# Performance work log

Measured on AMD Instinct MI355X. Metric: run time of the kernel, lower is better.

The kernel has to match this reference:

```python
import jax, jax.numpy as jnp
import numpy as np

N, H, W, C = 8, 64, 64, 256  # C//4 = 64 query channels, HW = 4096 attention size


def setup_inputs() -> dict:
    key = jax.random.key(0)
    k1, k2, k3, k4 = jax.random.split(key, 4)
    src_mask = jax.random.uniform(k1, (N, H, W), dtype=jnp.float32)
    src_feature = jax.random.normal(k2, (N, H, W, C), dtype=jnp.float32)
    ref_feature = jax.random.normal(k3, (N, H, W, C), dtype=jnp.float32)
    w_query = jax.random.normal(k4, (C, C // 4), dtype=jnp.float32) * 0.02  # 1x1 conv weight
    return {"src_mask": src_mask, "src_feature": src_feature,
            "ref_feature": ref_feature, "w_query": w_query}


def _apply_attention_map(att_map, features):
    n, h, w, c = features.shape
    pixels = features.reshape(n, h * w, c).transpose(0, 2, 1)  # (N, C, HW)
    att_out = jnp.einsum('ncp,npq->ncq', pixels, att_map)      # (N, C, HW)
    return att_out.reshape(n, h, w, c)


def reference(src_mask, src_feature, ref_feature, w_query):
    n, h, w, c = src_feature.shape
    # 1x1 conv (no bias): per-pixel channel projection C -> C//4
    query = jnp.einsum('nhwc,cd->nhwd', src_feature, w_query).reshape(n, h * w, -1)
    # full (HW x HW) attention map, softmax over keys
    att_map = jax.nn.softmax(jnp.einsum('npd,nqd->npq', query, query), axis=-1)
    # original module applies the map to src_feature twice (src_att and ref_att)
    att_out = _apply_attention_map(att_map, src_feature)
    src_att = att_out
    ref_att = att_out
    m = src_mask[..., None]  # (N, H, W, 1)
    ex_guide_flow = m * ref_att + (1.0 - m) * ref_feature
    return jnp.concatenate([ex_guide_flow, src_att], axis=-1)  # (N, H, W, 2C)
```

## Files before the change

kernel.cpp:

```cpp
#include <hip/hip_runtime.h>

typedef unsigned short u16;
typedef unsigned int u32;
typedef __attribute__((ext_vector_type(8))) __bf16 bf16x8;
typedef __attribute__((ext_vector_type(8))) _Float16 f16x8;
typedef __attribute__((ext_vector_type(4))) float f32x4;

__device__ __forceinline__ float b2f(u16 b) {
    union { u32 u; float f; } v; v.u = ((u32)b) << 16; return v.f;
}
__device__ __forceinline__ u16 f2bf(float f) {
    union { float f; u32 u; } v; v.f = f;
    u32 u = v.u;
    return (u16)((u + 0x7fffu + ((u >> 16) & 1u)) >> 16);
}
__device__ __forceinline__ u16 f2h(float f) {
    _Float16 h = (_Float16)f;
    return __builtin_bit_cast(u16, h);
}
__device__ __forceinline__ u32 pkbf2(float a, float b) {
    u16 x = __builtin_bit_cast(u16, (__bf16)a);
    u16 y = __builtin_bit_cast(u16, (__bf16)b);
    return (u32)x | ((u32)y << 16);
}
__device__ __forceinline__ bf16x8 ldg8b(const u16* p) {
    uint4 v = *(const uint4*)p;
    return __builtin_bit_cast(bf16x8, v);
}
__device__ __forceinline__ f16x8 ldg8h(const u16* p) {
    uint4 v = *(const uint4*)p;
    return __builtin_bit_cast(f16x8, v);
}
__device__ __forceinline__ f32x4 mfma_bf(bf16x8 a, bf16x8 b, f32x4 c) {
    return __builtin_amdgcn_mfma_f32_16x16x32_bf16(a, b, c, 0, 0, 0);
}
__device__ __forceinline__ f32x4 mfma_h(f16x8 a, f16x8 b, f32x4 c) {
    return __builtin_amdgcn_mfma_f32_16x16x32_f16(a, b, c, 0, 0, 0);
}

#define LOG2E 1.44269504088896340736f


__global__ void k0_wt(const float* __restrict__ Wq,
                      u16* __restrict__ Wthi, u16* __restrict__ Wtlo) {
    int idx = blockIdx.x * 256 + threadIdx.x;
    int c = idx >> 6, d = idx & 63;
    float w = Wq[idx];
    u16 hi = f2bf(w);
    float rem = w - b2f(hi);
    Wthi[d * 256 + c] = hi;
    Wtlo[d * 256 + c] = f2bf(rem);
}

__global__ __launch_bounds__(256) void k1_query(
    const float* __restrict__ F, const u16* __restrict__ Wthi,
    const u16* __restrict__ Wtlo, u16* __restrict__ Qh) {
    const int t = threadIdx.x;
    const int w = t >> 6, L = t & 63, lane16 = L & 15, quad = L >> 4;
    const int R0 = blockIdx.x * 64;
    const int row = R0 + w * 16 + lane16;
    const f32x4 z4 = {0.f, 0.f, 0.f, 0.f};
    f32x4 acc[4] = {z4, z4, z4, z4};
    union U8 { bf16x8 v; u16 s[8]; };
#pragma unroll
    for (int ks = 0; ks < 8; ++ks) {
        const float* fp = F + (size_t)row * 256 + ks * 32 + quad * 8;
        float4 x0 = *(const float4*)fp;
        float4 x1 = *(const float4*)(fp + 4);
        float xs[8] = {x0.x, x0.y, x0.z, x0.w, x1.x, x1.y, x1.z, x1.w};
        U8 ahi, alo;
#pragma unroll
        for (int j = 0; j < 8; ++j) {
            u16 h = f2bf(xs[j]);
            ahi.s[j] = h;
            alo.s[j] = f2bf(xs[j] - b2f(h));
        }
#pragma unroll
        for (int nt = 0; nt < 4; ++nt) {
            const int off = (nt * 16 + lane16) * 256 + ks * 32 + quad * 8;
            bf16x8 bh = ldg8b(Wthi + off);
            bf16x8 bl = ldg8b(Wtlo + off);
            acc[nt] = mfma_bf(ahi.v, bh, acc[nt]);
            acc[nt] = mfma_bf(alo.v, bh, acc[nt]);
            acc[nt] = mfma_bf(ahi.v, bl, acc[nt]);
        }
    }
    const int orow = R0 + w * 16 + quad * 4;
#pragma unroll
    for (int nt = 0; nt < 4; ++nt) {
        const int d = nt * 16 + lane16;
#pragma unroll
        for (int r = 0; r < 4; ++r) {
            const int p = orow + r;
            Qh[(size_t)p * 64 + (d ^ ((p & 7) << 3))] = f2h(acc[nt][r]);
        }
    }
}

__global__ __launch_bounds__(256) void k2_suminv(
    const u16* __restrict__ Q, float* __restrict__ lgl) {
    const int t = threadIdx.x;
    const int w = t >> 6, L = t & 63, lane16 = L & 15, quad = L >> 4, l7 = lane16 & 7;
    const int bx = blockIdx.x;
    const int n = bx & 7, pb = bx >> 3;
    const int P0 = pb * 32;
    const u16* Qn = Q + (size_t)n * 4096 * 64;

    f16x8 ap[2][2];
#pragma unroll
    for (int st = 0; st < 2; ++st) {
        const int row = P0 + st * 16 + lane16;
        ap[st][0] = ldg8h(Qn + row * 64 + ((quad * 8) ^ (l7 * 8)));
        ap[st][1] = ldg8h(Qn + row * 64 + ((32 + quad * 8) ^ (l7 * 8)));
    }
    float sums[2][4];
#pragma unroll
    for (int st = 0; st < 2; ++st)
#pragma unroll
        for (int r = 0; r < 4; ++r) sums[st][r] = 0.f;

    const f32x4 z4 = {0.f, 0.f, 0.f, 0.f};
    for (int s = 0; s < 32; ++s) {
#pragma unroll
        for (int nt = 0; nt < 2; ++nt) {
            const int qr = w * 1024 + s * 32 + nt * 16 + lane16;
            f16x8 b0 = ldg8h(Qn + qr * 64 + ((quad * 8) ^ (l7 * 8)));
            f16x8 b1 = ldg8h(Qn + qr * 64 + ((32 + quad * 8) ^ (l7 * 8)));
#pragma unroll
            for (int st = 0; st < 2; ++st) {
                f32x4 z = z4;
                z = mfma_h(ap[st][0], b0, z);
                z = mfma_h(ap[st][1], b1, z);
                sums[st][0] += __expf(z[0]);
                sums[st][1] += __expf(z[1]);
                sums[st][2] += __expf(z[2]);
                sums[st][3] += __expf(z[3]);
            }
        }
    }
    __shared__ float red[4][32];
#pragma unroll
    for (int st = 0; st < 2; ++st)
#pragma unroll
        for (int r = 0; r < 4; ++r) {
            float v = sums[st][r];
            v += __shfl_xor(v, 1);
            v += __shfl_xor(v, 2);
            v += __shfl_xor(v, 4);
            v += __shfl_xor(v, 8);
            if (lane16 == 0) red[w][st * 16 + quad * 4 + r] = v;
        }
    __syncthreads();
    if (t < 32) {
        float tot = red[0][t] + red[1][t] + red[2][t] + red[3][t];
        lgl[n * 4096 + P0 + t] = -__log2f(tot);
    }
}

__global__ __launch_bounds__(256) void k3_gt(
    const float* __restrict__ F, u16* __restrict__ Gt) {
    const int t = threadIdx.x;
    const int bx = blockIdx.x;
    const int n = bx >> 6, s = bx & 63;
    const int p0 = s * 64;
    __shared__ float tile[64][65];
    const float* Fn = F + (size_t)n * 4096 * 256;
    u16* Gn = Gt + (size_t)(n * 64 + s) * 16384;
#pragma unroll 1
    for (int ct = 0; ct < 4; ++ct) {
        const int c0 = ct * 64;
        if (ct > 0) __syncthreads();
#pragma unroll
        for (int k = 0; k < 16; ++k) {
            int idx = k * 256 + t;
            int r = idx >> 6, cc = idx & 63;
            tile[r][cc] = Fn[(size_t)(p0 + r) * 256 + c0 + cc];
        }
        __syncthreads();
#pragma unroll
        for (int k = 0; k < 2; ++k) {
            int u = k * 256 + t;
            int cc = u & 63, S = u >> 6;
            int G = S ^ (cc & 7);
            u16 v[8];
#pragma unroll
            for (int j = 0; j < 8; ++j) v[j] = f2bf(tile[G * 8 + j][cc]);
            uint4 pk;
            pk.x = (u32)v[0] | ((u32)v[1] << 16);
            pk.y = (u32)v[2] | ((u32)v[3] << 16);
            pk.z = (u32)v[4] | ((u32)v[5] << 16);
            pk.w = (u32)v[6] | ((u32)v[7] << 16);
            *(uint4*)&Gn[(c0 + cc) * 64 + S * 8] = pk;
        }
    }
}

__global__ __launch_bounds__(256, 2) void k4_attn(
    const u16* __restrict__ Q, const u16* __restrict__ Gt,
    const float* __restrict__ lgl, const float* __restrict__ mask,
    const float* __restrict__ ref, float* __restrict__ out) {
    const int t = threadIdx.x;
    const int w = t >> 6, L = t & 63, lane16 = L & 15, quad = L >> 4, l7 = lane16 & 7;
    const int bx = blockIdx.x;
    const int n = bx & 7, qb = bx >> 3;
    const int q0 = qb << 6;

    __shared__ u16 sP[2][4096];

    const u16* Qn = Q + (size_t)n * 4096 * 64;
    const u16* Gtn = Gt + (size_t)n * 64 * 16384;
    const float* iln = lgl + n * 4096;

    f16x8 bq[4][2];
#pragma unroll
    for (int qt = 0; qt < 4; ++qt) {
        const int row = q0 + qt * 16 + lane16;
        bq[qt][0] = ldg8h(Qn + row * 64 + ((quad * 8) ^ (l7 * 8)));
        bq[qt][1] = ldg8h(Qn + row * 64 + ((32 + quad * 8) ^ (l7 * 8)));
    }

    const int sAg0 = (w * 16 + lane16) * 64 + ((quad * 8) ^ (l7 * 8));
    const int sAg1 = (w * 16 + lane16) * 64 + ((32 + quad * 8) ^ (l7 * 8));
    int wrP[4];
#pragma unroll
    for (int qt = 0; qt < 4; ++qt)
        wrP[qt] = (qt * 16 + lane16) * 64 +
                  ((w * 16 + 8 * (quad >> 1)) ^ (l7 * 8)) + 4 * (quad & 1);
    int rdP[4][2], sOf[4][2];
#pragma unroll
    for (int m = 0; m < 4; ++m)
#pragma unroll
        for (int h = 0; h < 2; ++h)
            rdP[m][h] = (m * 16 + lane16) * 64 + ((h * 32 + quad * 8) ^ (l7 * 8));
#pragma unroll
    for (int nt = 0; nt < 4; ++nt)
#pragma unroll
        for (int h = 0; h < 2; ++h)
            sOf[nt][h] = (w * 64 + nt * 16 + lane16) * 64 + ((h * 32 + quad * 8) ^ (l7 * 8));

    const f32x4 z4 = {0.f, 0.f, 0.f, 0.f};
    f32x4 acc[4][4];
#pragma unroll
    for (int a = 0; a < 4; ++a)
#pragma unroll
        for (int b = 0; b < 4; ++b) acc[a][b] = z4;

    f16x8 na0, na1;
    float4 nil4;
    bf16x8 bbA[8], bbB[8];

    auto s_phase = [&](f16x8 a0, f16x8 a1, float4 il4, u16* dst) {
        float lg0 = il4.x, lg1 = il4.y, lg2 = il4.z, lg3 = il4.w;
#pragma unroll
        for (int qt = 0; qt < 4; ++qt) {
            f32x4 z = z4;
            z = mfma_h(a0, bq[qt][0], z);
            z = mfma_h(a1, bq[qt][1], z);
            uint2 pk;
            pk.x = pkbf2(__builtin_exp2f(__builtin_fmaf(z[0], LOG2E, lg0)),
                         __builtin_exp2f(__builtin_fmaf(z[1], LOG2E, lg1)));
            pk.y = pkbf2(__builtin_exp2f(__builtin_fmaf(z[2], LOG2E, lg2)),
                         __builtin_exp2f(__builtin_fmaf(z[3], LOG2E, lg3)));
            *(uint2*)&dst[wrP[qt]] = pk;
        }
    };
    auto load_bb = [&](const u16* gstep, bf16x8* bb) {
#pragma unroll
        for (int h = 0; h < 2; ++h)
#pragma unroll
            for (int nt = 0; nt < 4; ++nt)
                bb[h * 4 + nt] = ldg8b(gstep + sOf[nt][h]);
    };
    auto pv_phase = [&](const u16* sPc, const bf16x8* bb) {
        __builtin_amdgcn_s_setprio(1);
#pragma unroll
        for (int h = 0; h < 2; ++h) {
            bf16x8 af[4];
#pragma unroll
            for (int m = 0; m < 4; ++m) af[m] = ldg8b(&sPc[rdP[m][h]]);
#pragma unroll
            for (int nt = 0; nt < 4; ++nt)
#pragma unroll
                for (int m = 0; m < 4; ++m)
                    acc[m][nt] = mfma_bf(af[m], bb[h * 4 + nt], acc[m][nt]);
        }
        __builtin_amdgcn_s_setprio(0);
    };

    {
        f16x8 a0 = ldg8h(Qn + sAg0);
        f16x8 a1 = ldg8h(Qn + sAg1);
        float4 il4 = *(const float4*)(iln + w * 16 + quad * 4);
        s_phase(a0, a1, il4, &sP[0][0]);
    }
    __builtin_amdgcn_sched_barrier(0);
    na0 = ldg8h(Qn + 4096 + sAg0);
    na1 = ldg8h(Qn + 4096 + sAg1);
    nil4 = *(const float4*)(iln + 64 + w * 16 + quad * 4);
    __builtin_amdgcn_sched_barrier(0);
    load_bb(Gtn, bbA);
    __builtin_amdgcn_sched_barrier(0);
    asm volatile("s_waitcnt lgkmcnt(0)" ::: "memory");
    __builtin_amdgcn_s_barrier();

#pragma unroll 1
    for (int j = 0; j < 32; ++j) {
        const int i = 2 * j;
        s_phase(na0, na1, nil4, &sP[1][0]);
        __builtin_amdgcn_sched_barrier(0);
        if (i + 2 < 64) {
            na0 = ldg8h(Qn + (size_t)(i + 2) * 4096 + sAg0);
            na1 = ldg8h(Qn + (size_t)(i + 2) * 4096 + sAg1);
            nil4 = *(const float4*)(iln + (i + 2) * 64 + w * 16 + quad * 4);
        }
        __builtin_amdgcn_sched_barrier(0);
        load_bb(Gtn + (size_t)(i + 1) * 16384, bbB);
        __builtin_amdgcn_sched_barrier(0);
        pv_phase(&sP[0][0], bbA);
        asm volatile("s_waitcnt lgkmcnt(0)" ::: "memory");
        __builtin_amdgcn_s_barrier();

        if (i + 2 < 64) {
            s_phase(na0, na1, nil4, &sP[0][0]);
            __builtin_amdgcn_sched_barrier(0);
            if (i + 3 < 64) {
                na0 = ldg8h(Qn + (size_t)(i + 3) * 4096 + sAg0);
                na1 = ldg8h(Qn + (size_t)(i + 3) * 4096 + sAg1);
                nil4 = *(const float4*)(iln + (i + 3) * 64 + w * 16 + quad * 4);
            }
            __builtin_amdgcn_sched_barrier(0);
            load_bb(Gtn + (size_t)(i + 2) * 16384, bbA);
            __builtin_amdgcn_sched_barrier(0);
        }
        pv_phase(&sP[1][0], bbB);
        asm volatile("s_waitcnt lgkmcnt(0)" ::: "memory");
        __builtin_amdgcn_s_barrier();
    }

    const int tb = qb >> 2;
    const int cb = (qb & 3) * 64;
    const float* maskn = mask + n * 4096;
    const float* refn = ref + (size_t)n * 4096 * 256;
    float* outn = out + (size_t)n * 4096 * 512;
#pragma unroll
    for (int nt = 0; nt < 4; ++nt) {
        const int ch = w * 64 + nt * 16 + lane16;
        const int pixel = ch * 16 + tb;
        const float m = maskn[pixel];
#pragma unroll
        for (int mt = 0; mt < 4; ++mt) {
            const int c4 = cb + mt * 16 + quad * 4;
            float4 r4 = *(const float4*)(refn + (size_t)pixel * 256 + c4);
            float a0 = acc[mt][nt][0], a1 = acc[mt][nt][1];
            float a2 = acc[mt][nt][2], a3 = acc[mt][nt][3];
            float4 a4 = {a0, a1, a2, a3};
            float4 bl4 = {m * a0 + (1.f - m) * r4.x,
                          m * a1 + (1.f - m) * r4.y,
                          m * a2 + (1.f - m) * r4.z,
                          m * a3 + (1.f - m) * r4.w};
            *(float4*)(outn + (size_t)pixel * 512 + 256 + c4) = a4;
            *(float4*)(outn + (size_t)pixel * 512 + c4) = bl4;
        }
    }
}

extern "C" void kernel_launch(void* const* d_in, const int* in_sizes, int n_in,
                              void* d_out, int out_size, void* d_ws, size_t ws_size,
                              hipStream_t stream) {
    const float* mask = (const float*)d_in[0];
    const float* F    = (const float*)d_in[1];
    const float* ref  = (const float*)d_in[2];
    const float* Wq   = (const float*)d_in[3];
    float* out = (float*)d_out;
    char* ws = (char*)d_ws;

    u16*   Wthi = (u16*)ws;
    u16*   Wtlo = (u16*)(ws + 32768);
    u16*   Qh   = (u16*)(ws + 65536);
    float* lgl  = (float*)(ws + 65536 + 4194304);
    u16*   Gt   = (u16*)(ws + 65536 + 4194304 + 131072);

    k0_wt    <<<64,   256, 0, stream>>>(Wq, Wthi, Wtlo);
    k1_query <<<512,  256, 0, stream>>>(F, Wthi, Wtlo, Qh);
    k2_suminv<<<1024, 256, 0, stream>>>(Qh, lgl);
    k3_gt    <<<512,  256, 0, stream>>>(F, Gt);
    k4_attn  <<<512,  256, 0, stream>>>(Qh, Gt, lgl, mask, ref, out);
}
```

Baseline: 279.2 us.

## Hoist P-tile LDS reads before S-phase and drop sched barriers in attention loop

The attention main loop now reads both halves of the P fragments from shared memory at the start of each half-iteration, before issuing the next Q/G global loads and the S-phase softmax compute. The explicit sched_barrier fences are removed so the compiler can interleave LDS reads, global loads, exp work and MFMAs. The conversion helper is also switched to the hardware bf16 cast and packed pairs in the transpose kernel. Keeping all eight A fragments live raises register pressure, and removing the scheduling fences could let the compiler produce a worse schedule.

```diff
diff --git a/kernel.cpp b/kernel.cpp
--- a/kernel.cpp
+++ b/kernel.cpp
@@ -10,9 +10,7 @@
     union { u32 u; float f; } v; v.u = ((u32)b) << 16; return v.f;
 }
 __device__ __forceinline__ u16 f2bf(float f) {
-    union { float f; u32 u; } v; v.f = f;
-    u32 u = v.u;
-    return (u16)((u + 0x7fffu + ((u >> 16) & 1u)) >> 16);
+    return __builtin_bit_cast(u16, (__bf16)f);
 }
 __device__ __forceinline__ u16 f2h(float f) {
     _Float16 h = (_Float16)f;
@@ -182,14 +180,11 @@
             int u = k * 256 + t;
             int cc = u & 63, S = u >> 6;
             int G = S ^ (cc & 7);
-            u16 v[8];
-#pragma unroll
-            for (int j = 0; j < 8; ++j) v[j] = f2bf(tile[G * 8 + j][cc]);
             uint4 pk;
-            pk.x = (u32)v[0] | ((u32)v[1] << 16);
-            pk.y = (u32)v[2] | ((u32)v[3] << 16);
-            pk.z = (u32)v[4] | ((u32)v[5] << 16);
-            pk.w = (u32)v[6] | ((u32)v[7] << 16);
+            pk.x = pkbf2(tile[G * 8 + 0][cc], tile[G * 8 + 1][cc]);
+            pk.y = pkbf2(tile[G * 8 + 2][cc], tile[G * 8 + 3][cc]);
+            pk.z = pkbf2(tile[G * 8 + 4][cc], tile[G * 8 + 5][cc]);
+            pk.w = pkbf2(tile[G * 8 + 6][cc], tile[G * 8 + 7][cc]);
             *(uint4*)&Gn[(c0 + cc) * 64 + S * 8] = pk;
         }
     }
@@ -271,19 +266,21 @@
             for (int nt = 0; nt < 4; ++nt)
                 bb[h * 4 + nt] = ldg8b(gstep + sOf[nt][h]);
     };
-    auto pv_phase = [&](const u16* sPc, const bf16x8* bb) {
+    auto load_af = [&](const u16* sPc, bf16x8 af[2][4]) {
+#pragma unroll
+        for (int h = 0; h < 2; ++h)
+#pragma unroll
+            for (int m = 0; m < 4; ++m) af[h][m] = ldg8b(&sPc[rdP[m][h]]);
+    };
+    auto pv_phase = [&](bf16x8 af[2][4], const bf16x8* bb) {
         __builtin_amdgcn_s_setprio(1);
 #pragma unroll
-        for (int h = 0; h < 2; ++h) {
-            bf16x8 af[4];
-#pragma unroll
-            for (int m = 0; m < 4; ++m) af[m] = ldg8b(&sPc[rdP[m][h]]);
+        for (int h = 0; h < 2; ++h)
 #pragma unroll
             for (int nt = 0; nt < 4; ++nt)
 #pragma unroll
                 for (int m = 0; m < 4; ++m)
-                    acc[m][nt] = mfma_bf(af[m], bb[h * 4 + nt], acc[m][nt]);
-        }
+                    acc[m][nt] = mfma_bf(af[h][m], bb[h * 4 + nt], acc[m][nt]);
         __builtin_amdgcn_s_setprio(0);
     };
 
@@ -293,46 +290,49 @@
         float4 il4 = *(const float4*)(iln + w * 16 + quad * 4);
         s_phase(a0, a1, il4, &sP[0][0]);
     }
-    __builtin_amdgcn_sched_barrier(0);
     na0 = ldg8h(Qn + 4096 + sAg0);
     na1 = ldg8h(Qn + 4096 + sAg1);
     nil4 = *(const float4*)(iln + 64 + w * 16 + quad * 4);
-    __builtin_amdgcn_sched_barrier(0);
     load_bb(Gtn, bbA);
-    __builtin_amdgcn_sched_barrier(0);
     asm volatile("s_waitcnt lgkmcnt(0)" ::: "memory");
     __builtin_amdgcn_s_barrier();
 
 #pragma unroll 1
     for (int j = 0; j < 32; ++j) {
         const int i = 2 * j;
-        s_phase(na0, na1, nil4, &sP[1][0]);
-        __builtin_amdgcn_sched_barrier(0);
-        if (i + 2 < 64) {
-            na0 = ldg8h(Qn + (size_t)(i + 2) * 4096 + sAg0);
-            na1 = ldg8h(Qn + (size_t)(i + 2) * 4096 + sAg1);
-            nil4 = *(const float4*)(iln + (i + 2) * 64 + w * 16 + quad * 4);
-        }
-        __builtin_amdgcn_sched_barrier(0);
-        load_bb(Gtn + (size_t)(i + 1) * 16384, bbB);
-        __builtin_amdgcn_sched_barrier(0);
-        pv_phase(&sP[0][0], bbA);
+        {
+            bf16x8 af[2][4];
+            load_af(&sP[0][0], af);
+            f16x8 a0 = na0, a1 = na1;
+            float4 il = nil4;
+            if (i + 2 < 64) {
+                na0 = ldg8h(Qn + (size_t)(i + 2) * 4096 + sAg0);
+                na1 = ldg8h(Qn + (size_t)(i + 2) * 4096 + sAg1);
+                nil4 = *(const float4*)(iln + (i + 2) * 64 + w * 16 + quad * 4);
+            }
+            load_bb(Gtn + (size_t)(i + 1) * 16384, bbB);
+            s_phase(a0, a1, il, &sP[1][0]);
+            pv_phase(af, bbA);
+        }
         asm volatile("s_waitcnt lgkmcnt(0)" ::: "memory");
         __builtin_amdgcn_s_barrier();
 
-        if (i + 2 < 64) {
-            s_phase(na0, na1, nil4, &sP[0][0]);
-            __builtin_amdgcn_sched_barrier(0);
+        {
+            bf16x8 af[2][4];
+            load_af(&sP[1][0], af);
+            f16x8 a0 = na0, a1 = na1;
+            float4 il = nil4;
             if (i + 3 < 64) {
                 na0 = ldg8h(Qn + (size_t)(i + 3) * 4096 + sAg0);
                 na1 = ldg8h(Qn + (size_t)(i + 3) * 4096 + sAg1);
                 nil4 = *(const float4*)(iln + (i + 3) * 64 + w * 16 + quad * 4);
             }
-            __builtin_amdgcn_sched_barrier(0);
-            load_bb(Gtn + (size_t)(i + 2) * 16384, bbA);
-            __builtin_amdgcn_sched_barrier(0);
-        }
-        pv_phase(&sP[1][0], bbB);
+            if (i + 2 < 64) {
+                load_bb(Gtn + (size_t)(i + 2) * 16384, bbA);
+                s_phase(a0, a1, il, &sP[0][0]);
+            }
+            pv_phase(af, bbB);
+        }
         asm volatile("s_waitcnt lgkmcnt(0)" ::: "memory");
         __builtin_amdgcn_s_barrier();
     }
```

Measured after the change: 313.2 us. 1.12x slower.
